# Optimization experiments

Hardware: AMD Instinct MI355X
Metric: run time of the kernel (lower is better)

Reference implementation:

```python
import jax, jax.numpy as jnp
import numpy as np

NUM_HEADS = 16

def setup_inputs() -> dict:
    key = jax.random.key(0)
    k1, k2, k3 = jax.random.split(key, 3)
    B, N, C = 2, 2048, 1024
    x = jax.random.normal(k1, (B, N, C), dtype=jnp.float32)
    Wqkv = jax.random.normal(k2, (3 * C, C), dtype=jnp.float32) * (C ** -0.5)
    Wproj = jax.random.normal(k3, (C, C), dtype=jnp.float32) * (C ** -0.5)
    bproj = jnp.zeros((C,), dtype=jnp.float32)
    return {"x": x, "Wqkv": Wqkv, "Wproj": Wproj, "bproj": bproj}

def reference(x, Wqkv, Wproj, bproj):
    B, N, C = x.shape
    H = NUM_HEADS
    D = C // H
    scale = D ** -0.5
    # torch Linear: y = x @ W^T ; qkv -> [B,N,3,H,D]
    qkv = (x @ Wqkv.T).reshape(B, N, 3, H, D)
    q = qkv[:, :, 0].transpose(0, 2, 1, 3)  # [B,H,N,D]
    k = qkv[:, :, 1].transpose(0, 2, 1, 3)
    v = qkv[:, :, 2].transpose(0, 2, 1, 3)
    attn = jnp.einsum('bhnd,bhmd->bhnm', q, k) * scale  # [B,H,N,N]
    attn = jax.nn.softmax(attn, axis=-1)
    out = jnp.einsum('bhnm,bhmd->bhnd', attn, v)  # [B,H,N,D]
    out = out.transpose(0, 2, 1, 3).reshape(B, N, C)
    return out @ Wproj.T + bproj
```

## Files before the change

kernel.cpp:

```cpp
#include <hip/hip_runtime.h>

typedef unsigned short u16;
typedef unsigned int u32;
typedef __attribute__((ext_vector_type(8))) short short8;
typedef __attribute__((ext_vector_type(8))) __bf16 bf16x8;
typedef __attribute__((ext_vector_type(4))) float f32x4;
typedef __attribute__((ext_vector_type(16))) float f32x16;
typedef __attribute__((ext_vector_type(4))) unsigned short us4;
typedef __attribute__((ext_vector_type(4))) unsigned int u32x4;

#define DEVFN static __device__ __forceinline__

DEVFN u16 f2bf(float f) {
  u32 u = __float_as_uint(f);
  return (u16)((u + 0x7fffu + ((u >> 16) & 1u)) >> 16);
}

#if __has_builtin(__builtin_amdgcn_exp2f)
DEVFN float fexp2(float x) { return __builtin_amdgcn_exp2f(x); }
#else
DEVFN float fexp2(float x) { return exp2f(x); }
#endif

DEVFN float fmax3(float a, float b, float c) {
  return fmaxf(fmaxf(a, b), c);
}

template <typename T>
DEVFN auto mfma16_imp(T a, T b, f32x4 c, int)
    -> decltype(__builtin_amdgcn_mfma_f32_16x16x32_bf16(a, b, c, 0, 0, 0)) {
  return __builtin_amdgcn_mfma_f32_16x16x32_bf16(a, b, c, 0, 0, 0);
}
template <typename T>
DEVFN f32x4 mfma16_imp(T a, T b, f32x4 c, long) {
  return __builtin_amdgcn_mfma_f32_16x16x32_bf16(
      __builtin_bit_cast(bf16x8, a), __builtin_bit_cast(bf16x8, b), c, 0, 0, 0);
}
DEVFN f32x4 MFMA(short8 a, short8 b, f32x4 c) { return mfma16_imp(a, b, c, 0); }

template <typename T>
DEVFN auto mfma32_imp(T a, T b, f32x16 c, int)
    -> decltype(__builtin_amdgcn_mfma_f32_32x32x16_bf16(a, b, c, 0, 0, 0)) {
  return __builtin_amdgcn_mfma_f32_32x32x16_bf16(a, b, c, 0, 0, 0);
}
template <typename T>
DEVFN f32x16 mfma32_imp(T a, T b, f32x16 c, long) {
  return __builtin_amdgcn_mfma_f32_32x32x16_bf16(
      __builtin_bit_cast(bf16x8, a), __builtin_bit_cast(bf16x8, b), c, 0, 0, 0);
}
DEVFN f32x16 MFMA32(short8 a, short8 b, f32x16 c) { return mfma32_imp(a, b, c, 0); }

DEVFN void gload_lds16(const u16* g, u16* l) {
  __builtin_amdgcn_global_load_lds(
      (__attribute__((address_space(1))) void*)g,
      (__attribute__((address_space(3))) void*)l, 16, 0, 0);
}

DEVFN u32 cvtpk_bf16(float lo, float hi) {
  u32 w;
  asm("v_cvt_pk_bf16_f32 %0, %1, %2" : "=v"(w) : "v"(lo), "v"(hi));
  return w;
}

__global__ void __launch_bounds__(256) cvt_all(
    const float* __restrict__ x, u16* __restrict__ xo,
    const float* __restrict__ w1, u16* __restrict__ w1o,
    const float* __restrict__ w2, u16* __restrict__ w2o) {
  int bid = blockIdx.x;
  const float* in;
  u16* out;
  int i;
  if (bid < 4096) {
    in = x; out = xo; i = bid * 256 + threadIdx.x;
  } else if (bid < 7168) {
    in = w1; out = w1o; i = (bid - 4096) * 256 + threadIdx.x;
  } else {
    in = w2; out = w2o; i = (bid - 7168) * 256 + threadIdx.x;
  }
  f32x4 v = ((const f32x4*)in)[i];
  us4 o;
  o[0] = f2bf(v[0]); o[1] = f2bf(v[1]); o[2] = f2bf(v[2]); o[3] = f2bf(v[3]);
  ((us4*)out)[i] = o;
}

template <int F32OUT, int BN>
DEVFN void gemm_tile(const u16* __restrict__ A, const u16* __restrict__ Bm,
                     u16* __restrict__ Cbf, float* __restrict__ Cf,
                     const float* __restrict__ bias, int N, int K, int bm,
                     int bn, u16* As, u16* Bs) {
  const int tid = threadIdx.x;
  const int wave = tid >> 6, lane = tid & 63;
  const int wr = (wave >> 1) * 64, wc = (wave & 1) * (BN / 2);
  const int srow = lane >> 2, scol = (lane & 3) * 8;
  const int fr = lane & 15, fk = (lane >> 4) * 8;
  const int NB = BN / 64;
  const int NI = BN / 32;

  f32x4 acc[4][NI] = {};

  for (int k0 = 0; k0 < K; k0 += 32) {
    __syncthreads();
#pragma unroll
    for (int t = 0; t < 2; ++t) {
      int rr = (wave * 2 + t) * 16 + srow;
      gload_lds16(A + (size_t)(bm + rr) * K + k0 + scol, As + (wave * 2 + t) * 512);
    }
#pragma unroll
    for (int t = 0; t < NB; ++t) {
      int rr = (wave * NB + t) * 16 + srow;
      gload_lds16(Bm + (size_t)(bn + rr) * K + k0 + scol, Bs + (wave * NB + t) * 512);
    }
    __syncthreads();
    short8 af[4], bf[NI];
#pragma unroll
    for (int i = 0; i < 4; ++i)
      af[i] = *(const short8*)(As + (wr + i * 16 + fr) * 32 + fk);
#pragma unroll
    for (int i = 0; i < NI; ++i)
      bf[i] = *(const short8*)(Bs + (wc + i * 16 + fr) * 32 + fk);
#pragma unroll
    for (int mi = 0; mi < 4; ++mi)
#pragma unroll
      for (int ni = 0; ni < NI; ++ni)
        acc[mi][ni] = MFMA(af[mi], bf[ni], acc[mi][ni]);
  }

  const int orow = (lane >> 4) * 4, ocol = lane & 15;
#pragma unroll
  for (int mi = 0; mi < 4; ++mi)
#pragma unroll
    for (int ni = 0; ni < NI; ++ni)
#pragma unroll
      for (int r = 0; r < 4; ++r) {
        size_t row = (size_t)(bm + wr + mi * 16 + orow + r);
        size_t col = (size_t)(bn + wc + ni * 16 + ocol);
        if (F32OUT)
          Cf[row * N + col] = acc[mi][ni][r] + bias[col];
        else
          Cbf[row * N + col] = f2bf(acc[mi][ni][r]);
      }
}

__global__ void __launch_bounds__(256) gemm_proj(
    const u16* __restrict__ A, const u16* __restrict__ Bm,
    float* __restrict__ Cf, const float* __restrict__ bias, int M, int N,
    int K) {
  __shared__ u16 As[128 * 32];
  __shared__ u16 Bs[64 * 32];
  const int B = blockIdx.x;
  const int L = (B & 7) * 64 + (B >> 3);
  gemm_tile<1, 64>(A, Bm, nullptr, Cf, bias, N, K, (L >> 4) * 128,
                   (L & 15) * 64, As, Bs);
}

DEVFN void gemm_tile64(const u16* __restrict__ A, const u16* __restrict__ Bm,
                       u16* __restrict__ C, int N, int K, int bm, int bn,
                       u16* As, u16* Bs) {
  const int tid = threadIdx.x;
  const int wave = tid >> 6, lane = tid & 63;
  const int wr = (wave >> 1) * 64, wc = (wave & 1) * 64;
  const int rowl = lane >> 3;
  const int scol = ((lane & 7) ^ rowl) * 8;
  const int fr = lane & 15, fkc = lane >> 4;

  f32x4 acc[4][4] = {};

  for (int k0 = 0; k0 < K; k0 += 64) {
    __syncthreads();
#pragma unroll
    for (int t = 0; t < 4; ++t) {
      int gA = wave * 4 + t;
      int row = gA * 8 + rowl;
      gload_lds16(A + (size_t)(bm + row) * K + k0 + scol, As + gA * 512);
      gload_lds16(Bm + (size_t)(bn + row) * K + k0 + scol, Bs + gA * 512);
    }
    __syncthreads();
#pragma unroll
    for (int ks = 0; ks < 2; ++ks) {
      short8 af[4], bf[4];
#pragma unroll
      for (int i = 0; i < 4; ++i) {
        int ra = wr + i * 16 + fr, rb = wc + i * 16 + fr;
        int lc = fkc + ks * 4;
        af[i] = *(const short8*)(As + ra * 64 + ((lc ^ (ra & 7)) * 8));
        bf[i] = *(const short8*)(Bs + rb * 64 + ((lc ^ (rb & 7)) * 8));
      }
#pragma unroll
      for (int mi = 0; mi < 4; ++mi)
#pragma unroll
        for (int ni = 0; ni < 4; ++ni)
          acc[mi][ni] = MFMA(af[mi], bf[ni], acc[mi][ni]);
    }
  }

  const int orow = (lane >> 4) * 4, ocol = lane & 15;
#pragma unroll
  for (int mi = 0; mi < 4; ++mi)
#pragma unroll
    for (int ni = 0; ni < 4; ++ni)
#pragma unroll
      for (int r = 0; r < 4; ++r) {
        size_t row = (size_t)(bm + wr + mi * 16 + orow + r);
        size_t col = (size_t)(bn + wc + ni * 16 + ocol);
        C[row * N + col] = f2bf(acc[mi][ni][r]);
      }
}

__global__ void __launch_bounds__(256) fused_qkv_gemm(
    const u16* __restrict__ x, const u16* __restrict__ wqkv,
    u16* __restrict__ qk, u16* __restrict__ vt) {
  __shared__ u16 As[128 * 64];
  __shared__ u16 Bs[128 * 64];
  const int B = blockIdx.x;
  const int L = (B & 7) * 96 + (B >> 3);
  if (L < 512) {
    gemm_tile64(x, wqkv, qk, 2048, 1024, (L >> 4) * 128, (L & 15) * 128,
                As, Bs);
  } else {
    int j = L - 512;
    gemm_tile64(wqkv + (size_t)2048 * 1024, x, vt, 4096, 1024, (j & 7) * 128,
                (j >> 3) * 128, As, Bs);
  }
}

__global__ void __launch_bounds__(512) attn_kernel(const u16* __restrict__ qk,
                                                   const u16* __restrict__ vT,
                                                   u16* __restrict__ attn_out) {
  __shared__ u16 SM[32768];

  const int tid = threadIdx.x;
  const int wave = tid >> 6, lane = tid & 63;
  const int g = wave >> 2, gw = wave & 3;
  const int q5 = lane & 31, hi = lane >> 5;

  const int B = blockIdx.x;
  const int L = (B & 7) * 64 + (B >> 3);
  const int qb = L & 15, hb = L >> 4;
  const int h = hb & 15, b = hb >> 4;

  const size_t tok0 = (size_t)b * 2048;
  const float SCALE = 0.18033688011112042f;

  u16* const Kg = SM + g * 2 * 4096;
  u16* const Vg = SM + 16384 + g * 2 * 4096;
  const int kvoff = g * 1024;

  const size_t qrow = tok0 + qb * 128 + gw * 32 + q5;
  const u16* qp = qk + qrow * 2048 + h * 64 + hi * 8;
  short8 qf[4];
#pragma unroll
  for (int ks = 0; ks < 4; ++ks) qf[ks] = *(const short8*)(qp + ks * 16);

  const u16* kbase = qk + tok0 * 2048 + 1024 + h * 64;
  const u16* vtb = vT + (size_t)h * 64 * 4096 + tok0;

  const int rowl = lane >> 3;
  const int k_srcoff = ((lane & 7) ^ rowl) * 8;

  float m_run = -1e30f, l_run = 0.f;
  f32x16 o0 = {}, o1 = {};

#define STAGE(kv0, buf)                                                        \
  {                                                                            \
    _Pragma("unroll") for (int c = 0; c < 2; ++c) {                            \
      int rw = c * 4 + gw;                                                     \
      int row = rw * 8 + rowl;                                                 \
      gload_lds16(kbase + (size_t)((kv0) + row) * 2048 + k_srcoff,             \
                  Kg + (buf) * 4096 + rw * 512);                               \
      int vso = (((lane & 7) ^ rowl ^ rw) * 8);    \
      gload_lds16(vtb + (size_t)row * 4096 + (kv0) + vso,                      \
                  Vg + (buf) * 4096 + rw * 512);                               \
    }                                                                          \
  }

  STAGE(kvoff, 0);
  __syncthreads();

  for (int t = 0; t < 16; ++t) {
    const int cur = t & 1, nxt = cur ^ 1;
    if (t < 15) STAGE(kvoff + (t + 1) * 64, nxt);

    const u16* Kc = Kg + cur * 4096;
    f32x16 s0 = {}, s1 = {};
    __builtin_amdgcn_s_setprio(1);
#pragma unroll
    for (int ks = 0; ks < 4; ++ks) {
      int ch = ((ks * 2 + hi) ^ (q5 & 7)) * 8;
      short8 k0 = *(const short8*)(Kc + q5 * 64 + ch);
      short8 k1 = *(const short8*)(Kc + (32 + q5) * 64 + ch);
      s0 = MFMA32(k0, qf[ks], s0);
      s1 = MFMA32(k1, qf[ks], s1);
    }
    __builtin_amdgcn_s_setprio(0);

    float m0 = fmax3(s0[0], s0[1], s0[2]);
    float m1 = fmax3(s0[3], s0[4], s0[5]);
    float m2 = fmax3(s0[6], s0[7], s0[8]);
    float m3 = fmax3(s0[9], s0[10], s0[11]);
    float m4 = fmax3(s0[12], s0[13], s0[14]);
    float m5 = fmax3(s0[15], s1[0], s1[1]);
    float m6 = fmax3(s1[2], s1[3], s1[4]);
    float m7 = fmax3(s1[5], s1[6], s1[7]);
    float m8 = fmax3(s1[8], s1[9], s1[10]);
    float m9 = fmax3(s1[11], s1[12], s1[13]);
    float ma = fmaxf(s1[14], s1[15]);
    float n0 = fmax3(m0, m1, m2);
    float n1 = fmax3(m3, m4, m5);
    float n2 = fmax3(m6, m7, m8);
    float n3 = fmax3(m9, ma, n0);
    float pmax = fmax3(n1, n2, n3);
    pmax = fmaxf(pmax, __shfl_xor(pmax, 32, 64));
    float mraw = pmax * SCALE;

    if (__any(mraw > m_run + 8.f)) {
      float mn = fmaxf(m_run, mraw);
      float alpha = fexp2(m_run - mn);
#pragma unroll
      for (int i = 0; i < 16; ++i) { o0[i] *= alpha; o1[i] *= alpha; }
      l_run *= alpha;
      m_run = mn;
    }

    float p0[16], p1[16];
    float rs = 0.f;
#pragma unroll
    for (int i = 0; i < 16; ++i) {
      p0[i] = fexp2(fmaf(s0[i], SCALE, -m_run));
      p1[i] = fexp2(fmaf(s1[i], SCALE, -m_run));
      rs += p0[i] + p1[i];
    }
    l_run += rs;

    u32 w0[4][2], w1[4][2];
#pragma unroll
    for (int a = 0; a < 4; ++a) {
      w0[a][0] = cvtpk_bf16(p0[4 * a], p0[4 * a + 1]);
      w0[a][1] = cvtpk_bf16(p0[4 * a + 2], p0[4 * a + 3]);
      w1[a][0] = cvtpk_bf16(p1[4 * a], p1[4 * a + 1]);
      w1[a][1] = cvtpk_bf16(p1[4 * a + 2], p1[4 * a + 3]);
    }
    short8 pb[4];
#pragma unroll
    for (int ks = 0; ks < 4; ++ks) {
      int e = ks & 1;
      u32 x0 = (ks < 2) ? w0[2 * e][0] : w1[2 * e][0];
      u32 y0 = (ks < 2) ? w0[2 * e + 1][0] : w1[2 * e + 1][0];
      u32 x1 = (ks < 2) ? w0[2 * e][1] : w1[2 * e][1];
      u32 y1 = (ks < 2) ? w0[2 * e + 1][1] : w1[2 * e + 1][1];
      asm("v_permlane32_swap_b32 %0, %1" : "+v"(x0), "+v"(y0));
      asm("v_permlane32_swap_b32 %0, %1" : "+v"(x1), "+v"(y1));
      u32x4 tt = {x0, x1, y0, y1};
      pb[ks] = __builtin_bit_cast(short8, tt);
    }

    const u16* Vc = Vg + cur * 4096;
    __builtin_amdgcn_s_setprio(1);
#pragma unroll
    for (int ks = 0; ks < 4; ++ks) {
      int ch0 = ((ks * 2 + hi) ^ (q5 & 7) ^ ((q5 >> 3) & 7)) * 8;
      int ch1 = ch0 ^ (4 * 8);
      short8 v0 = *(const short8*)(Vc + q5 * 64 + ch0);
      short8 v1 = *(const short8*)(Vc + (32 + q5) * 64 + ch1);
      o0 = MFMA32(v0, pb[ks], o0);
      o1 = MFMA32(v1, pb[ks], o1);
    }
    __builtin_amdgcn_s_setprio(0);

    __syncthreads();
  }
#undef STAGE

  l_run += __shfl_xor(l_run, 32, 64);

  float* sm = (float*)SM;
  float* base = sm + gw * 2176;
  if (g == 1) {
    base[lane] = m_run;
    base[64 + lane] = l_run;
#pragma unroll
    for (int i = 0; i < 16; ++i) {
      base[128 + i * 64 + lane] = o0[i];
      base[128 + (16 + i) * 64 + lane] = o1[i];
    }
  }
  __syncthreads();
  if (g == 0) {
    float m1 = base[lane], l1 = base[64 + lane];
    float M = fmaxf(m_run, m1);
    float wa = fexp2(m_run - M), wb = fexp2(m1 - M);
    float inv = 1.f / (wa * l_run + wb * l1);
#pragma unroll
    for (int dt = 0; dt < 2; ++dt)
#pragma unroll
      for (int gq = 0; gq < 4; ++gq) {
        us4 st;
#pragma unroll
        for (int c2 = 0; c2 < 4; ++c2) {
          int i = 4 * gq + c2;
          float mine = (dt == 0) ? o0[i] : o1[i];
          float oth = base[128 + (dt * 16 + i) * 64 + lane];
          st[c2] = f2bf((wa * mine + wb * oth) * inv);
        }
        int col = h * 64 + dt * 32 + 8 * gq + 4 * hi;
        *(us4*)(attn_out + qrow * 1024 + col) = st;
      }
  }
}

extern "C" void kernel_launch(void* const* d_in, const int* in_sizes, int n_in,
                              void* d_out, int out_size, void* d_ws, size_t ws_size,
                              hipStream_t stream) {
  const float* x = (const float*)d_in[0];
  const float* Wqkv = (const float*)d_in[1];
  const float* Wproj = (const float*)d_in[2];
  const float* bproj = (const float*)d_in[3];
  float* out = (float*)d_out;

  char* ws = (char*)d_ws;
  u16* x_bf     = (u16*)(ws);
  u16* wqkv_bf  = (u16*)(ws + 8388608);
  u16* wproj_bf = (u16*)(ws + 14680064);
  u16* qk_bf    = (u16*)(ws + 16777216);
  u16* vt_bf    = (u16*)(ws + 33554432);
  u16* attn_bf  = (u16*)(ws + 41943040);

  cvt_all<<<8192, 256, 0, stream>>>(x, x_bf, Wqkv, wqkv_bf, Wproj, wproj_bf);

  fused_qkv_gemm<<<768, 256, 0, stream>>>(x_bf, wqkv_bf, qk_bf, vt_bf);

  attn_kernel<<<512, 512, 0, stream>>>(qk_bf, vt_bf, attn_bf);

  gemm_proj<<<512, 256, 0, stream>>>(attn_bf, wproj_bf, out, bproj,
                                     4096, 1024, 1024);
}
```

Before: 117.1 us.

## Split attention KV range across four wave groups with 1024-thread blocks

The attention kernel now launches 1024 threads per block, so four wave groups each handle a quarter of the KV sequence instead of two groups each handling half. This raises parallelism and shortens each group's serial loop. To fit LDS, the double-buffered K/V staging is dropped in favour of a single buffer loaded at the top of each iteration, followed by a barrier, so loads no longer overlap compute. The partial softmax states are then combined through a tree merge in shared memory, which adds barriers and costs register headroom at the larger block size.

```diff
diff --git a/kernel.cpp b/kernel.cpp
--- a/kernel.cpp
+++ b/kernel.cpp
@@ -223,9 +223,9 @@
   }
 }
 
-__global__ void __launch_bounds__(512) attn_kernel(const u16* __restrict__ qk,
-                                                   const u16* __restrict__ vT,
-                                                   u16* __restrict__ attn_out) {
+__global__ void __launch_bounds__(1024, 8) attn_kernel(
+    const u16* __restrict__ qk, const u16* __restrict__ vT,
+    u16* __restrict__ attn_out) {
   __shared__ u16 SM[32768];
 
   const int tid = threadIdx.x;
@@ -241,9 +241,9 @@
   const size_t tok0 = (size_t)b * 2048;
   const float SCALE = 0.18033688011112042f;
 
-  u16* const Kg = SM + g * 2 * 4096;
-  u16* const Vg = SM + 16384 + g * 2 * 4096;
-  const int kvoff = g * 1024;
+  u16* const Kg = SM + g * 4096;
+  u16* const Vg = SM + 16384 + g * 4096;
+  const int kvoff = g * 512;
 
   const size_t qrow = tok0 + qb * 128 + gw * 32 + q5;
   const u16* qp = qk + qrow * 2048 + h * 64 + hi * 8;
@@ -260,34 +260,29 @@
   float m_run = -1e30f, l_run = 0.f;
   f32x16 o0 = {}, o1 = {};
 
-#define STAGE(kv0, buf)                                                        \
+#define STAGE(kv0)                                                             \
   {                                                                            \
     _Pragma("unroll") for (int c = 0; c < 2; ++c) {                            \
       int rw = c * 4 + gw;                                                     \
       int row = rw * 8 + rowl;                                                 \
       gload_lds16(kbase + (size_t)((kv0) + row) * 2048 + k_srcoff,             \
-                  Kg + (buf) * 4096 + rw * 512);                               \
+                  Kg + rw * 512);                                              \
       int vso = (((lane & 7) ^ rowl ^ rw) * 8);    \
-      gload_lds16(vtb + (size_t)row * 4096 + (kv0) + vso,                      \
-                  Vg + (buf) * 4096 + rw * 512);                               \
+      gload_lds16(vtb + (size_t)row * 4096 + (kv0) + vso, Vg + rw * 512);      \
     }                                                                          \
   }
 
-  STAGE(kvoff, 0);
-  __syncthreads();
-
-  for (int t = 0; t < 16; ++t) {
-    const int cur = t & 1, nxt = cur ^ 1;
-    if (t < 15) STAGE(kvoff + (t + 1) * 64, nxt);
-
-    const u16* Kc = Kg + cur * 4096;
+  for (int t = 0; t < 8; ++t) {
+    STAGE(kvoff + t * 64);
+    __syncthreads();
+
     f32x16 s0 = {}, s1 = {};
     __builtin_amdgcn_s_setprio(1);
 #pragma unroll
     for (int ks = 0; ks < 4; ++ks) {
       int ch = ((ks * 2 + hi) ^ (q5 & 7)) * 8;
-      short8 k0 = *(const short8*)(Kc + q5 * 64 + ch);
-      short8 k1 = *(const short8*)(Kc + (32 + q5) * 64 + ch);
+      short8 k0 = *(const short8*)(Kg + q5 * 64 + ch);
+      short8 k1 = *(const short8*)(Kg + (32 + q5) * 64 + ch);
       s0 = MFMA32(k0, qf[ks], s0);
       s1 = MFMA32(k1, qf[ks], s1);
     }
@@ -353,14 +348,13 @@
       pb[ks] = __builtin_bit_cast(short8, tt);
     }
 
-    const u16* Vc = Vg + cur * 4096;
     __builtin_amdgcn_s_setprio(1);
 #pragma unroll
     for (int ks = 0; ks < 4; ++ks) {
       int ch0 = ((ks * 2 + hi) ^ (q5 & 7) ^ ((q5 >> 3) & 7)) * 8;
       int ch1 = ch0 ^ (4 * 8);
-      short8 v0 = *(const short8*)(Vc + q5 * 64 + ch0);
-      short8 v1 = *(const short8*)(Vc + (32 + q5) * 64 + ch1);
+      short8 v0 = *(const short8*)(Vg + q5 * 64 + ch0);
+      short8 v1 = *(const short8*)(Vg + (32 + q5) * 64 + ch1);
       o0 = MFMA32(v0, pb[ks], o0);
       o1 = MFMA32(v1, pb[ks], o1);
     }
@@ -372,9 +366,8 @@
 
   l_run += __shfl_xor(l_run, 32, 64);
 
-  float* sm = (float*)SM;
-  float* base = sm + gw * 2176;
-  if (g == 1) {
+  float* const base = (float*)SM + gw * 2176;
+  auto writeP = [&]() {
     base[lane] = m_run;
     base[64 + lane] = l_run;
 #pragma unroll
@@ -382,13 +375,33 @@
       base[128 + i * 64 + lane] = o0[i];
       base[128 + (16 + i) * 64 + lane] = o1[i];
     }
-  }
+  };
+  auto mergeP = [&]() {
+    float mo = base[lane], lo_ = base[64 + lane];
+    float M = fmaxf(m_run, mo);
+    float wa = fexp2(m_run - M), wb = fexp2(mo - M);
+    l_run = wa * l_run + wb * lo_;
+#pragma unroll
+    for (int i = 0; i < 16; ++i) {
+      o0[i] = wa * o0[i] + wb * base[128 + i * 64 + lane];
+      o1[i] = wa * o1[i] + wb * base[128 + (16 + i) * 64 + lane];
+    }
+    m_run = M;
+  };
+
+  if (g == 1) writeP();
+  __syncthreads();
+  if (g == 0) mergeP();
+  __syncthreads();
+  if (g == 3) writeP();
+  __syncthreads();
+  if (g == 2) mergeP();
+  __syncthreads();
+  if (g == 2) writeP();
   __syncthreads();
   if (g == 0) {
-    float m1 = base[lane], l1 = base[64 + lane];
-    float M = fmaxf(m_run, m1);
-    float wa = fexp2(m_run - M), wb = fexp2(m1 - M);
-    float inv = 1.f / (wa * l_run + wb * l1);
+    mergeP();
+    float inv = 1.f / l_run;
 #pragma unroll
     for (int dt = 0; dt < 2; ++dt)
 #pragma unroll
@@ -397,9 +410,8 @@
 #pragma unroll
         for (int c2 = 0; c2 < 4; ++c2) {
           int i = 4 * gq + c2;
-          float mine = (dt == 0) ? o0[i] : o1[i];
-          float oth = base[128 + (dt * 16 + i) * 64 + lane];
-          st[c2] = f2bf((wa * mine + wb * oth) * inv);
+          float val = (dt == 0 ? o0[i] : o1[i]) * inv;
+          st[c2] = f2bf(val);
         }
         int col = h * 64 + dt * 32 + 8 * gq + 4 * hi;
         *(us4*)(attn_out + qrow * 1024 + col) = st;
@@ -428,7 +440,7 @@
 
   fused_qkv_gemm<<<768, 256, 0, stream>>>(x_bf, wqkv_bf, qk_bf, vt_bf);
 
-  attn_kernel<<<512, 512, 0, stream>>>(qk_bf, vt_bf, attn_bf);
+  attn_kernel<<<512, 1024, 0, stream>>>(qk_bf, vt_bf, attn_bf);
 
   gemm_proj<<<512, 256, 0, stream>>>(attn_bf, wproj_bf, out, bproj,
                                      4096, 1024, 1024);
```

Result: slower. 399.8 us (+241.4%).
